# Performance work log

Measured on AMD Instinct MI355X. Metric: run time of the kernel, lower is better.

Reference implementation:

```python
import jax, jax.numpy as jnp
import numpy as np

B, S, D, H = 4, 2048, 1024, 16
HD = D // H  # head_dim = 64


def setup_inputs() -> dict:
    key = jax.random.key(0)
    ks = jax.random.split(key, 11)
    s = 1.0 / np.sqrt(D)
    return {
        "Q": jax.random.normal(ks[0], (B, S, D), dtype=jnp.float32),
        "K": jax.random.normal(ks[1], (B, S, D), dtype=jnp.float32),
        "V": jax.random.normal(ks[2], (B, S, D), dtype=jnp.float32),
        "Wq": jax.random.normal(ks[3], (D, D), dtype=jnp.float32) * s,
        "bq": jnp.zeros((D,), dtype=jnp.float32),
        "Wk": jax.random.normal(ks[4], (D, D), dtype=jnp.float32) * s,
        "bk": jnp.zeros((D,), dtype=jnp.float32),
        "Wv": jax.random.normal(ks[5], (D, D), dtype=jnp.float32) * s,
        "bv": jnp.zeros((D,), dtype=jnp.float32),
        "Wo": jax.random.normal(ks[6], (D, D), dtype=jnp.float32) * s,
        "bo": jnp.zeros((D,), dtype=jnp.float32),
    }


def _split_heads(x):
    # [B, S, D] -> [B, H, S, HD]
    b, s, _ = x.shape
    return x.reshape(b, s, H, HD).transpose(0, 2, 1, 3)


def reference(Q, K, V, Wq, bq, Wk, bk, Wv, bv, Wo, bo):
    q = _split_heads(Q @ Wq + bq)  # [B,H,S,HD]
    k = _split_heads(K @ Wk + bk)
    v = _split_heads(V @ Wv + bv)
    scale = 1.0 / jnp.sqrt(jnp.float32(HD))
    scores = jnp.einsum('bhqd,bhkd->bhqk', q, k) * scale  # [B,H,S,S]
    attn = jax.nn.softmax(scores, axis=-1)
    out = jnp.einsum('bhqk,bhkd->bhqd', attn, v)  # [B,H,S,HD]
    out = out.transpose(0, 2, 1, 3).reshape(Q.shape[0], -1, D)  # [B,S,D]
    return out @ Wo + bo
```

## Files before the change

### kernel.cpp

```cpp
#include <hip/hip_runtime.h>
#include <hip/hip_bf16.h>

typedef unsigned short u16;
typedef unsigned int u32;
typedef u16 u16x4 __attribute__((ext_vector_type(4)));
typedef u16 u16x8 __attribute__((ext_vector_type(8)));
typedef u32 u32x4 __attribute__((ext_vector_type(4)));
typedef float f32x4 __attribute__((ext_vector_type(4)));
typedef float f32x16 __attribute__((ext_vector_type(16)));
typedef __bf16 bf16x8 __attribute__((ext_vector_type(8)));

#define MFMA16(A, B, C) __builtin_amdgcn_mfma_f32_16x16x32_bf16( \
    __builtin_bit_cast(bf16x8, (A)), __builtin_bit_cast(bf16x8, (B)), (C), 0, 0, 0)
#define MFMA32(A, B, C) __builtin_amdgcn_mfma_f32_32x32x16_bf16( \
    __builtin_bit_cast(bf16x8, (A)), __builtin_bit_cast(bf16x8, (B)), (C), 0, 0, 0)

__device__ __forceinline__ u16 f2bf(float f) {
    u32 u = __float_as_uint(f);
    u += 0x7fffu + ((u >> 16) & 1u);
    return (u16)(u >> 16);
}

__device__ __forceinline__ u32 cvtpk(float lo, float hi) {
    u32 d;
    asm("v_cvt_pk_bf16_f32 %0, %1, %2" : "=v"(d) : "v"(lo), "v"(hi));
    return d;
}

__device__ __forceinline__ void gll16(const void* g, void* l) {
    __builtin_amdgcn_global_load_lds(
        (const __attribute__((address_space(1))) void*)g,
        (__attribute__((address_space(3))) void*)l, 16, 0, 0);
}

__global__ void f2bf3(const float* __restrict__ a0, const float* __restrict__ a1,
                      const float* __restrict__ a2, u16* __restrict__ o0,
                      u16* __restrict__ o1, u16* __restrict__ o2, int n4) {
    const float* in = (blockIdx.y == 0) ? a0 : (blockIdx.y == 1) ? a1 : a2;
    u16* out = (blockIdx.y == 0) ? o0 : (blockIdx.y == 1) ? o1 : o2;
    int i = blockIdx.x * blockDim.x + threadIdx.x;
    int stride = gridDim.x * blockDim.x;
    for (; i < n4; i += stride) {
        float4 v = ((const float4*)in)[i];
        u16x4 o;
        o[0] = f2bf(v.x); o[1] = f2bf(v.y); o[2] = f2bf(v.z); o[3] = f2bf(v.w);
        ((u16x4*)out)[i] = o;
    }
}

__global__ void cvt_wt(const float* __restrict__ W0, const float* __restrict__ W1,
                       const float* __restrict__ W2, const float* __restrict__ W3,
                       u16* __restrict__ T0, u16* __restrict__ T1,
                       u16* __restrict__ T2, u16* __restrict__ T3) {
    const int z = blockIdx.z;
    const float* W = (z == 0) ? W0 : (z == 1) ? W1 : (z == 2) ? W2 : W3;
    u16* T = (z == 0) ? T0 : (z == 1) ? T1 : (z == 2) ? T2 : T3;
    __shared__ float tile[64][65];
    const int n0 = blockIdx.x * 64, k0 = blockIdx.y * 64;
    const int tx = threadIdx.x & 63, ty = threadIdx.x >> 6;
#pragma unroll
    for (int i = 0; i < 16; ++i) {
        int r = i * 4 + ty;
        tile[r][tx] = W[(size_t)(k0 + r) * 1024 + n0 + tx];
    }
    __syncthreads();
#pragma unroll
    for (int i = 0; i < 16; ++i) {
        int r = i * 4 + ty;
        T[(size_t)(n0 + r) * 1024 + k0 + tx] = f2bf(tile[tx][r]);
    }
}

__device__ __forceinline__ void gemm_core(
    const u16* __restrict__ A, const u16* __restrict__ Bt,
    const float* __restrict__ bias, void* __restrict__ out,
    int mode, float scale, int bm, int bn, u16* lAs, u16* lBs) {
    const int tid = threadIdx.x, lane = tid & 63, wid = tid >> 6;
    const int wr = wid >> 1, wc = wid & 1;
    const int l15 = lane & 15, l16 = lane >> 4;

    f32x4 acc[4][4];
#pragma unroll
    for (int i = 0; i < 4; ++i)
#pragma unroll
        for (int j = 0; j < 4; ++j) acc[i][j] = f32x4{0.f, 0.f, 0.f, 0.f};

    const char* Ab = (const char*)A;
    const char* Bb = (const char*)Bt;
    char* ldsA = (char*)lAs;
    char* ldsB = (char*)lBs;
    const int rA0 = wid * 32 + (lane >> 3);
    const int ci = ((lane & 7) ^ (lane >> 3)) * 16;

    for (int k0 = 0; k0 < 1024; k0 += 64) {
        __syncthreads();
#pragma unroll
        for (int c = 0; c < 4; ++c) {
            int row = rA0 + c * 8;
            gll16(Ab + ((size_t)(bm + row) * 1024 + k0) * 2 + ci, ldsA + (wid * 4 + c) * 1024);
            gll16(Bb + ((size_t)(bn + row) * 1024 + k0) * 2 + ci, ldsB + (wid * 4 + c) * 1024);
        }
        asm volatile("s_waitcnt vmcnt(0)" ::: "memory");
        __syncthreads();

#pragma unroll
        for (int kk = 0; kk < 2; ++kk) {
            u16x8 af[4], bf[4];
#pragma unroll
            for (int mi = 0; mi < 4; ++mi) {
                int row = wr * 64 + mi * 16 + l15;
                int cg = kk * 4 + l16;
                af[mi] = *(const u16x8*)(ldsA + row * 128 + ((cg ^ (row & 7)) * 16));
            }
#pragma unroll
            for (int ni = 0; ni < 4; ++ni) {
                int row = wc * 64 + ni * 16 + l15;
                int cg = kk * 4 + l16;
                bf[ni] = *(const u16x8*)(ldsB + row * 128 + ((cg ^ (row & 7)) * 16));
            }
#pragma unroll
            for (int mi = 0; mi < 4; ++mi)
#pragma unroll
                for (int ni = 0; ni < 4; ++ni)
                    acc[mi][ni] = MFMA16(af[mi], bf[ni], acc[mi][ni]);
        }
    }

    const int row0 = bm + wr * 64, col0 = bn + wc * 64;
#pragma unroll
    for (int ni = 0; ni < 4; ++ni) {
        int col = col0 + ni * 16 + l15;
        float bv = bias[col];
#pragma unroll
        for (int mi = 0; mi < 4; ++mi) {
            int rowb = row0 + mi * 16 + l16 * 4;
            if (mode == 1) {
                int b = rowb >> 11, s = rowb & 2047, h = col >> 6, d = col & 63;
                u16x4 pv;
#pragma unroll
                for (int r = 0; r < 4; ++r) pv[r] = f2bf((acc[mi][ni][r] + bv) * scale);
                *(u16x4*)((u16*)out + (((size_t)(b * 16 + h)) * 64 + d) * 2048 + s) = pv;
            } else {
#pragma unroll
                for (int r = 0; r < 4; ++r) {
                    int row = rowb + r;
                    float v = (acc[mi][ni][r] + bv) * scale;
                    if (mode == 2) {
                        ((float*)out)[(size_t)row * 1024 + col] = v;
                    } else {
                        int b = row >> 11, s = row & 2047, h = col >> 6, d = col & 63;
                        ((u16*)out)[(((size_t)(b * 16 + h)) * 2048 + s) * 64 + d] = f2bf(v);
                    }
                }
            }
        }
    }
}

__device__ __forceinline__ void xcd_decode(int wg, int& bm, int& bn) {
    int xcd = wg & 7, pos = wg >> 3;
    bm = (xcd * 8 + (pos >> 3)) * 128;
    bn = (pos & 7) * 128;
}

__global__ __launch_bounds__(256, 3) void gemm_qkv(
    const u16* __restrict__ XQ, const u16* __restrict__ XK, const u16* __restrict__ XV,
    const u16* __restrict__ WQ, const u16* __restrict__ WK, const u16* __restrict__ WV,
    const float* __restrict__ bq, const float* __restrict__ bk, const float* __restrict__ bv,
    u16* __restrict__ qo, u16* __restrict__ ko, u16* __restrict__ vo, float qscale) {
    __shared__ u16 lAs[128 * 64];
    __shared__ u16 lBs[128 * 64];
    const int z = blockIdx.z;
    const u16* A = (z == 0) ? XQ : (z == 1) ? XK : XV;
    const u16* Bt = (z == 0) ? WQ : (z == 1) ? WK : WV;
    const float* bias = (z == 0) ? bq : (z == 1) ? bk : bv;
    u16* out = (z == 0) ? qo : (z == 1) ? ko : vo;
    const int mode = (z == 2) ? 1 : 0;
    const float scale = (z == 0) ? qscale : 1.0f;
    int bm, bn;
    xcd_decode(blockIdx.y * 8 + blockIdx.x, bm, bn);
    gemm_core(A, Bt, bias, out, mode, scale, bm, bn, lAs, lBs);
}

__global__ __launch_bounds__(256, 3) void gemm_out(
    const u16* __restrict__ A, const u16* __restrict__ Bt,
    const float* __restrict__ bias, float* __restrict__ out) {
    __shared__ u16 lAs[128 * 64];
    __shared__ u16 lBs[128 * 64];
    int bm, bn;
    xcd_decode(blockIdx.y * 8 + blockIdx.x, bm, bn);
    gemm_core(A, Bt, bias, out, 2, 1.0f, bm, bn, lAs, lBs);
}

__global__ __launch_bounds__(512, 2) void attn_fwd(
    const u16* __restrict__ qh, const u16* __restrict__ kh,
    const u16* __restrict__ vth, u16* __restrict__ ao) {
    __shared__ u16 lK[2][64 * 64];
    __shared__ u16 lV[2][64 * 64];
    const int tid = threadIdx.x, lane = tid & 63, wid = tid >> 6;
    const int l31 = lane & 31, l32 = lane >> 5;
    const int wg = blockIdx.x;
    const int xcd = wg & 7, pos = wg >> 3;
    const int bh = xcd * 8 + (pos >> 3);
    const int xblk = pos & 7;
    const int q0 = xblk * 256 + wid * 32;
    const char* kb = (const char*)(kh + (size_t)bh * 2048 * 64);
    const char* vb = (const char*)(vth + (size_t)bh * 64 * 2048);
    const u16* qb = qh + (size_t)bh * 2048 * 64;

    u16x8 qf[4];
#pragma unroll
    for (int kc = 0; kc < 4; ++kc)
        qf[kc] = *(const u16x8*)(qb + (size_t)(q0 + l31) * 64 + kc * 16 + l32 * 8);

    float l_run = 0.f;
    f32x16 oacc[2] = {};

    char* ldsK = (char*)lK;
    char* ldsV = (char*)lV;
    const int srow = wid * 8 + (lane >> 3);
    const int sci = ((lane & 7) ^ (lane >> 3)) * 16;

#define STAGE(kv0, bo) do { \
    gll16(kb + (size_t)((kv0) + srow) * 128 + sci, ldsK + (bo) + wid * 1024); \
    gll16(vb + (size_t)srow * 4096 + (size_t)(kv0) * 2 + sci, ldsV + (bo) + wid * 1024); \
} while (0)

    STAGE(0, 0);
    int cur = 0;

    for (int it = 0; it < 32; ++it) {
        if (it < 31) {
            STAGE((it + 1) * 64, (cur ^ 1) * 8192);
            asm volatile("s_waitcnt vmcnt(2)" ::: "memory");
        } else {
            asm volatile("s_waitcnt vmcnt(0)" ::: "memory");
        }
        __syncthreads();
        const char* K_ = ldsK + cur * 8192;
        const char* V_ = ldsV + cur * 8192;

        f32x16 s[2] = {};
        __builtin_amdgcn_s_setprio(1);
#pragma unroll
        for (int kc = 0; kc < 4; ++kc) {
#pragma unroll
            for (int sub = 0; sub < 2; ++sub) {
                int row = sub * 32 + l31;
                int cg = kc * 2 + l32;
                u16x8 kf = *(const u16x8*)(K_ + row * 128 + ((cg ^ (row & 7)) * 16));
                s[sub] = MFMA32(kf, qf[kc], s[sub]);
            }
        }
        __builtin_amdgcn_s_setprio(0);

        float p0[16], p1[16];
#pragma unroll
        for (int r = 0; r < 16; ++r) p0[r] = __builtin_amdgcn_exp2f(s[0][r]);
#pragma unroll
        for (int r = 0; r < 16; ++r) p1[r] = __builtin_amdgcn_exp2f(s[1][r]);

        u16x8 pa[2][2];
#pragma unroll
        for (int c2 = 0; c2 < 2; ++c2) {
            u32 x0 = cvtpk(p0[c2 * 8 + 0], p0[c2 * 8 + 1]);
            u32 x1 = cvtpk(p0[c2 * 8 + 2], p0[c2 * 8 + 3]);
            u32 y0 = cvtpk(p0[c2 * 8 + 4], p0[c2 * 8 + 5]);
            u32 y1 = cvtpk(p0[c2 * 8 + 6], p0[c2 * 8 + 7]);
            asm("v_permlane32_swap_b32 %0, %1" : "+v"(x0), "+v"(y0));
            asm("v_permlane32_swap_b32 %0, %1" : "+v"(x1), "+v"(y1));
            u32x4 wa = {x0, x1, y0, y1};
            pa[0][c2] = __builtin_bit_cast(u16x8, wa);
            u32 z0 = cvtpk(p1[c2 * 8 + 0], p1[c2 * 8 + 1]);
            u32 z1 = cvtpk(p1[c2 * 8 + 2], p1[c2 * 8 + 3]);
            u32 v0 = cvtpk(p1[c2 * 8 + 4], p1[c2 * 8 + 5]);
            u32 v1 = cvtpk(p1[c2 * 8 + 6], p1[c2 * 8 + 7]);
            asm("v_permlane32_swap_b32 %0, %1" : "+v"(z0), "+v"(v0));
            asm("v_permlane32_swap_b32 %0, %1" : "+v"(z1), "+v"(v1));
            u32x4 wb = {z0, z1, v0, v1};
            pa[1][c2] = __builtin_bit_cast(u16x8, wb);
        }

        float a8[8];
#pragma unroll
        for (int i = 0; i < 8; ++i)
            a8[i] = (p0[i] + p0[i + 8]) + (p1[i] + p1[i + 8]);
        float ls = ((a8[0] + a8[4]) + (a8[1] + a8[5])) +
                   ((a8[2] + a8[6]) + (a8[3] + a8[7]));
        ls += __shfl_xor(ls, 32);
        l_run += ls;

        __builtin_amdgcn_s_setprio(1);
#pragma unroll
        for (int dsub = 0; dsub < 2; ++dsub) {
#pragma unroll
            for (int sub = 0; sub < 2; ++sub) {
#pragma unroll
                for (int c2 = 0; c2 < 2; ++c2) {
                    int row = dsub * 32 + l31;
                    int cg = sub * 4 + c2 * 2 + l32;
                    u16x8 vf = *(const u16x8*)(V_ + row * 128 + ((cg ^ (row & 7)) * 16));
                    oacc[dsub] = MFMA32(pa[sub][c2], vf, oacc[dsub]);
                }
            }
        }
        __builtin_amdgcn_s_setprio(0);
        __syncthreads();
        cur ^= 1;
    }
#undef STAGE

    const int b = bh >> 4, h = bh & 15;
    float inv = 1.f / l_run;
#pragma unroll
    for (int r = 0; r < 16; ++r) {
        int rq = ((r & 3) + 8 * (r >> 2)) + 4 * l32;
        float fr = __shfl(inv, rq);
        int sq = q0 + rq;
#pragma unroll
        for (int dsub = 0; dsub < 2; ++dsub) {
            int d = dsub * 32 + l31;
            ao[((size_t)(b * 2048 + sq)) * 1024 + h * 64 + d] = f2bf(oacc[dsub][r] * fr);
        }
    }
}

extern "C" void kernel_launch(void* const* d_in, const int* in_sizes, int n_in,
                              void* d_out, int out_size, void* d_ws, size_t ws_size,
                              hipStream_t stream) {
    const float* Q  = (const float*)d_in[0];
    const float* K  = (const float*)d_in[1];
    const float* V  = (const float*)d_in[2];
    const float* Wq = (const float*)d_in[3];
    const float* bq = (const float*)d_in[4];
    const float* Wk = (const float*)d_in[5];
    const float* bk = (const float*)d_in[6];
    const float* Wv = (const float*)d_in[7];
    const float* bv = (const float*)d_in[8];
    const float* Wo = (const float*)d_in[9];
    const float* bo = (const float*)d_in[10];

    char* ws = (char*)d_ws;
    const size_t MB = 1024u * 1024u;
    u16* XQ  = (u16*)(ws);
    u16* XK  = (u16*)(ws + 16 * MB);
    u16* XV  = (u16*)(ws + 32 * MB);
    u16* WTQ = (u16*)(ws + 48 * MB);
    u16* WTK = (u16*)(ws + 50 * MB);
    u16* WTV = (u16*)(ws + 52 * MB);
    u16* WTO = (u16*)(ws + 54 * MB);
    u16* qhp = (u16*)(ws + 56 * MB);
    u16* khp = (u16*)(ws + 72 * MB);
    u16* vtp = (u16*)(ws + 88 * MB);
    u16* aop = XQ;

    const float qscale = 0.125f * 1.44269504088896f;

    cvt_wt<<<dim3(16, 16, 4), 256, 0, stream>>>(Wq, Wk, Wv, Wo, WTQ, WTK, WTV, WTO);
    f2bf3<<<dim3(2048, 3), 256, 0, stream>>>(Q, K, V, XQ, XK, XV, 2097152);

    gemm_qkv<<<dim3(8, 64, 3), 256, 0, stream>>>(XQ, XK, XV, WTQ, WTK, WTV,
                                                 bq, bk, bv, qhp, khp, vtp, qscale);

    attn_fwd<<<512, 512, 0, stream>>>(qhp, khp, vtp, aop);

    gemm_out<<<dim3(8, 64), 256, 0, stream>>>(aop, WTO, bo, (float*)d_out);
}
```

Measured before the change: 181.6 us.

## Process two 32-row query groups per wave in attention, halving block threads

Each wave in the attention kernel now handles 64 query rows (two 32-row groups) instead of 32, with 256 threads per block instead of 512. Every K/V fragment read from LDS feeds twice as many MFMAs, and each thread issues two staging loads per tile. The aim is fewer LDS reads per MFMA. The cost is roughly double the accumulator and score registers per wave and half the waves per block, which may lower occupancy and latency hiding.

After: 181.5 us. Within noise of the previous version (-0.1%).

```diff
diff --git a/kernel.cpp b/kernel.cpp
--- a/kernel.cpp
+++ b/kernel.cpp
@@ -192,7 +192,7 @@
     gemm_core(A, Bt, bias, out, 2, 1.0f, bm, bn, lAs, lBs);
 }
 
-__global__ __launch_bounds__(512, 2) void attn_fwd(
+__global__ __launch_bounds__(256, 2) void attn_fwd(
     const u16* __restrict__ qh, const u16* __restrict__ kh,
     const u16* __restrict__ vth, u16* __restrict__ ao) {
     __shared__ u16 lK[2][64 * 64];
@@ -203,28 +203,33 @@
     const int xcd = wg & 7, pos = wg >> 3;
     const int bh = xcd * 8 + (pos >> 3);
     const int xblk = pos & 7;
-    const int q0 = xblk * 256 + wid * 32;
+    const int q0 = xblk * 256 + wid * 64;
     const char* kb = (const char*)(kh + (size_t)bh * 2048 * 64);
     const char* vb = (const char*)(vth + (size_t)bh * 64 * 2048);
     const u16* qb = qh + (size_t)bh * 2048 * 64;
 
-    u16x8 qf[4];
-#pragma unroll
-    for (int kc = 0; kc < 4; ++kc)
-        qf[kc] = *(const u16x8*)(qb + (size_t)(q0 + l31) * 64 + kc * 16 + l32 * 8);
-
-    float l_run = 0.f;
-    f32x16 oacc[2] = {};
+    u16x8 qf[2][4];
+#pragma unroll
+    for (int qg = 0; qg < 2; ++qg)
+#pragma unroll
+        for (int kc = 0; kc < 4; ++kc)
+            qf[qg][kc] = *(const u16x8*)(qb + (size_t)(q0 + qg * 32 + l31) * 64 + kc * 16 + l32 * 8);
+
+    float l_run[2] = {0.f, 0.f};
+    f32x16 oacc[2][2] = {};
 
     char* ldsK = (char*)lK;
     char* ldsV = (char*)lV;
-    const int srow = wid * 8 + (lane >> 3);
+    const int srow = wid * 16 + (lane >> 3);
     const int sci = ((lane & 7) ^ (lane >> 3)) * 16;
 
 #define STAGE(kv0, bo) do { \
-    gll16(kb + (size_t)((kv0) + srow) * 128 + sci, ldsK + (bo) + wid * 1024); \
-    gll16(vb + (size_t)srow * 4096 + (size_t)(kv0) * 2 + sci, ldsV + (bo) + wid * 1024); \
-} while (0)
+    _Pragma("unroll") \
+    for (int c = 0; c < 2; ++c) { \
+        int row = srow + c * 8; \
+        gll16(kb + (size_t)((kv0) + row) * 128 + sci, ldsK + (bo) + (wid * 2 + c) * 1024); \
+        gll16(vb + (size_t)row * 4096 + (size_t)(kv0) * 2 + sci, ldsV + (bo) + (wid * 2 + c) * 1024); \
+    } } while (0)
 
     STAGE(0, 0);
     int cur = 0;
@@ -232,7 +237,7 @@
     for (int it = 0; it < 32; ++it) {
         if (it < 31) {
             STAGE((it + 1) * 64, (cur ^ 1) * 8192);
-            asm volatile("s_waitcnt vmcnt(2)" ::: "memory");
+            asm volatile("s_waitcnt vmcnt(4)" ::: "memory");
         } else {
             asm volatile("s_waitcnt vmcnt(0)" ::: "memory");
         }
@@ -240,7 +245,7 @@
         const char* K_ = ldsK + cur * 8192;
         const char* V_ = ldsV + cur * 8192;
 
-        f32x16 s[2] = {};
+        f32x16 s[2][2] = {};
         __builtin_amdgcn_s_setprio(1);
 #pragma unroll
         for (int kc = 0; kc < 4; ++kc) {
@@ -249,46 +254,48 @@
                 int row = sub * 32 + l31;
                 int cg = kc * 2 + l32;
                 u16x8 kf = *(const u16x8*)(K_ + row * 128 + ((cg ^ (row & 7)) * 16));
-                s[sub] = MFMA32(kf, qf[kc], s[sub]);
+                s[0][sub] = MFMA32(kf, qf[0][kc], s[0][sub]);
+                s[1][sub] = MFMA32(kf, qf[1][kc], s[1][sub]);
             }
         }
         __builtin_amdgcn_s_setprio(0);
 
-        float p0[16], p1[16];
-#pragma unroll
-        for (int r = 0; r < 16; ++r) p0[r] = __builtin_amdgcn_exp2f(s[0][r]);
-#pragma unroll
-        for (int r = 0; r < 16; ++r) p1[r] = __builtin_amdgcn_exp2f(s[1][r]);
-
-        u16x8 pa[2][2];
-#pragma unroll
-        for (int c2 = 0; c2 < 2; ++c2) {
-            u32 x0 = cvtpk(p0[c2 * 8 + 0], p0[c2 * 8 + 1]);
-            u32 x1 = cvtpk(p0[c2 * 8 + 2], p0[c2 * 8 + 3]);
-            u32 y0 = cvtpk(p0[c2 * 8 + 4], p0[c2 * 8 + 5]);
-            u32 y1 = cvtpk(p0[c2 * 8 + 6], p0[c2 * 8 + 7]);
-            asm("v_permlane32_swap_b32 %0, %1" : "+v"(x0), "+v"(y0));
-            asm("v_permlane32_swap_b32 %0, %1" : "+v"(x1), "+v"(y1));
-            u32x4 wa = {x0, x1, y0, y1};
-            pa[0][c2] = __builtin_bit_cast(u16x8, wa);
-            u32 z0 = cvtpk(p1[c2 * 8 + 0], p1[c2 * 8 + 1]);
-            u32 z1 = cvtpk(p1[c2 * 8 + 2], p1[c2 * 8 + 3]);
-            u32 v0 = cvtpk(p1[c2 * 8 + 4], p1[c2 * 8 + 5]);
-            u32 v1 = cvtpk(p1[c2 * 8 + 6], p1[c2 * 8 + 7]);
-            asm("v_permlane32_swap_b32 %0, %1" : "+v"(z0), "+v"(v0));
-            asm("v_permlane32_swap_b32 %0, %1" : "+v"(z1), "+v"(v1));
-            u32x4 wb = {z0, z1, v0, v1};
-            pa[1][c2] = __builtin_bit_cast(u16x8, wb);
-        }
-
-        float a8[8];
-#pragma unroll
-        for (int i = 0; i < 8; ++i)
-            a8[i] = (p0[i] + p0[i + 8]) + (p1[i] + p1[i + 8]);
-        float ls = ((a8[0] + a8[4]) + (a8[1] + a8[5])) +
-                   ((a8[2] + a8[6]) + (a8[3] + a8[7]));
-        ls += __shfl_xor(ls, 32);
-        l_run += ls;
+        u16x8 pa[2][2][2];
+#pragma unroll
+        for (int qg = 0; qg < 2; ++qg) {
+            float p0[16], p1[16];
+#pragma unroll
+            for (int r = 0; r < 16; ++r) p0[r] = __builtin_amdgcn_exp2f(s[qg][0][r]);
+#pragma unroll
+            for (int r = 0; r < 16; ++r) p1[r] = __builtin_amdgcn_exp2f(s[qg][1][r]);
+#pragma unroll
+            for (int c2 = 0; c2 < 2; ++c2) {
+                u32 x0 = cvtpk(p0[c2 * 8 + 0], p0[c2 * 8 + 1]);
+                u32 x1 = cvtpk(p0[c2 * 8 + 2], p0[c2 * 8 + 3]);
+                u32 y0 = cvtpk(p0[c2 * 8 + 4], p0[c2 * 8 + 5]);
+                u32 y1 = cvtpk(p0[c2 * 8 + 6], p0[c2 * 8 + 7]);
+                asm("v_permlane32_swap_b32 %0, %1" : "+v"(x0), "+v"(y0));
+                asm("v_permlane32_swap_b32 %0, %1" : "+v"(x1), "+v"(y1));
+                u32x4 wa = {x0, x1, y0, y1};
+                pa[qg][0][c2] = __builtin_bit_cast(u16x8, wa);
+                u32 z0 = cvtpk(p1[c2 * 8 + 0], p1[c2 * 8 + 1]);
+                u32 z1 = cvtpk(p1[c2 * 8 + 2], p1[c2 * 8 + 3]);
+                u32 v0 = cvtpk(p1[c2 * 8 + 4], p1[c2 * 8 + 5]);
+                u32 v1 = cvtpk(p1[c2 * 8 + 6], p1[c2 * 8 + 7]);
+                asm("v_permlane32_swap_b32 %0, %1" : "+v"(z0), "+v"(v0));
+                asm("v_permlane32_swap_b32 %0, %1" : "+v"(z1), "+v"(v1));
+                u32x4 wb = {z0, z1, v0, v1};
+                pa[qg][1][c2] = __builtin_bit_cast(u16x8, wb);
+            }
+            float a8[8];
+#pragma unroll
+            for (int i = 0; i < 8; ++i)
+                a8[i] = (p0[i] + p0[i + 8]) + (p1[i] + p1[i + 8]);
+            float ls = ((a8[0] + a8[4]) + (a8[1] + a8[5])) +
+                       ((a8[2] + a8[6]) + (a8[3] + a8[7]));
+            ls += __shfl_xor(ls, 32);
+            l_run[qg] += ls;
+        }
 
         __builtin_amdgcn_s_setprio(1);
 #pragma unroll
@@ -300,7 +307,8 @@
                     int row = dsub * 32 + l31;
                     int cg = sub * 4 + c2 * 2 + l32;
                     u16x8 vf = *(const u16x8*)(V_ + row * 128 + ((cg ^ (row & 7)) * 16));
-                    oacc[dsub] = MFMA32(pa[sub][c2], vf, oacc[dsub]);
+                    oacc[0][dsub] = MFMA32(pa[0][sub][c2], vf, oacc[0][dsub]);
+                    oacc[1][dsub] = MFMA32(pa[1][sub][c2], vf, oacc[1][dsub]);
                 }
             }
         }
@@ -311,16 +319,19 @@
 #undef STAGE
 
     const int b = bh >> 4, h = bh & 15;
-    float inv = 1.f / l_run;
-#pragma unroll
-    for (int r = 0; r < 16; ++r) {
-        int rq = ((r & 3) + 8 * (r >> 2)) + 4 * l32;
-        float fr = __shfl(inv, rq);
-        int sq = q0 + rq;
-#pragma unroll
-        for (int dsub = 0; dsub < 2; ++dsub) {
-            int d = dsub * 32 + l31;
-            ao[((size_t)(b * 2048 + sq)) * 1024 + h * 64 + d] = f2bf(oacc[dsub][r] * fr);
+#pragma unroll
+    for (int qg = 0; qg < 2; ++qg) {
+        float inv = 1.f / l_run[qg];
+#pragma unroll
+        for (int r = 0; r < 16; ++r) {
+            int rq = ((r & 3) + 8 * (r >> 2)) + 4 * l32;
+            float fr = __shfl(inv, rq);
+            int sq = q0 + qg * 32 + rq;
+#pragma unroll
+            for (int dsub = 0; dsub < 2; ++dsub) {
+                int d = dsub * 32 + l31;
+                ao[((size_t)(b * 2048 + sq)) * 1024 + h * 64 + d] = f2bf(oacc[qg][dsub][r] * fr);
+            }
         }
     }
 }
@@ -362,7 +373,7 @@
     gemm_qkv<<<dim3(8, 64, 3), 256, 0, stream>>>(XQ, XK, XV, WTQ, WTK, WTV,
                                                  bq, bk, bv, qhp, khp, vtp, qscale);
 
-    attn_fwd<<<512, 512, 0, stream>>>(qhp, khp, vtp, aop);
+    attn_fwd<<<512, 256, 0, stream>>>(qhp, khp, vtp, aop);
 
     gemm_out<<<dim3(8, 64), 256, 0, stream>>>(aop, WTO, bo, (float*)d_out);
 }
```
